# Kernel optimization log

Hardware: AMD Instinct MI355X
Metric: run time of the kernel (lower is better)

The kernel has to match this reference:

```python
import jax, jax.numpy as jnp
import numpy as np

B, S, D, H = 2, 2048, 2048, 16
HD = D // H          # 128, even for RoPE
GS = 0.1             # governance_strength
ROPE_BASE = 10000.0


def _rope_cos_sin(seq_len, dtype):
    # inv_freq over pairs of dims: [HD/2]
    inv_freq = 1.0 / (ROPE_BASE ** (jnp.arange(0, HD, 2, dtype=jnp.float32) / HD))
    t = jnp.arange(seq_len, dtype=jnp.float32)
    freqs = jnp.outer(t, inv_freq)          # [S, HD/2]
    return jnp.cos(freqs).astype(dtype), jnp.sin(freqs).astype(dtype)


def _apply_rope(x, cos, sin):
    # x: [B,H,S,HD]; cos/sin: [S,HD/2] -> broadcast over batch/heads
    x1, x2 = jnp.split(x, 2, axis=-1)
    c = cos[None, None, :, :]
    s = sin[None, None, :, :]
    return jnp.concatenate([x1 * c - x2 * s, x2 * c + x1 * s], axis=-1)


def setup_inputs() -> dict:
    key = jax.random.key(0)
    ks = jax.random.split(key, 8)
    sc = 1.0 / np.sqrt(D)
    return {
        "x": jax.random.normal(ks[0], (B, S, D), jnp.float32),
        "Wq": jax.random.normal(ks[1], (D, D), jnp.float32) * sc,
        "Wk": jax.random.normal(ks[2], (D, D), jnp.float32) * sc,
        "Wv": jax.random.normal(ks[3], (D, D), jnp.float32) * sc,
        "Wo": jax.random.normal(ks[4], (D, D), jnp.float32) * sc,
        "bo": jnp.zeros((D,), jnp.float32),
        "policy_mask": jax.random.uniform(ks[5], (1, H, S, S), jnp.float32),
        "memory_weights": jax.random.uniform(ks[6], (B, 1, 1, S), jnp.float32),
    }


def reference(x, Wq, Wk, Wv, Wo, bo, policy_mask, memory_weights):
    dtype = x.dtype
    scale = HD ** -0.5

    def heads(t):
        return t.reshape(B, S, H, HD).transpose(0, 2, 1, 3)  # [B,H,S,HD]

    q = heads(x @ Wq)
    k = heads(x @ Wk)
    v = heads(x @ Wv)

    cos, sin = _rope_cos_sin(S, dtype)
    q = _apply_rope(q, cos, sin)
    k = _apply_rope(k, cos, sin)

    scores = jnp.einsum("bhqd,bhkd->bhqk", q, k) * scale  # [B,H,S,S]

    # governance bias: policy term + memory-aware log term
    bias = policy_mask * GS + jnp.log1p(memory_weights * GS + 1e-8)
    scores = scores + bias

    # causal mask (no KV cache: kv_len == q_len)
    causal = jnp.tril(jnp.ones((S, S), bool))[None, None]
    scores = jnp.where(causal, scores, jnp.asarray(-1e9, dtype))

    attn = jax.nn.softmax(scores, axis=-1)
    out = jnp.einsum("bhqk,bhkd->bhqd", attn, v)          # [B,H,S,HD]
    out = out.transpose(0, 2, 1, 3).reshape(B, S, D)
    return out @ Wo + bo
```

## Files before the change

### kernel.cpp

```cpp
#include <hip/hip_runtime.h>
#include <hip/hip_bf16.h>
#include <math.h>

#define B_ 2
#define S_ 2048
#define D_ 2048
#define H_ 16
#define HD_ 128
#define NT_ (B_*S_)
#define GS_ 0.1f

typedef _Float16 half8 __attribute__((__vector_size__(16)));
typedef _Float16 half4v __attribute__((__vector_size__(8)));
typedef float f32x4 __attribute__((__vector_size__(16)));

__device__ __forceinline__ void gload_lds16(const void* g, void* s) {
  __builtin_amdgcn_global_load_lds(
      (const __attribute__((address_space(1))) unsigned int*)g,
      (__attribute__((address_space(3))) unsigned int*)s, 16, 0, 0);
}


__global__ void cvt_f32_to_f16(const float* __restrict__ in, _Float16* __restrict__ out, int n4) {
  int i = blockIdx.x * blockDim.x + threadIdx.x;
  if (i >= n4) return;
  float4 v = ((const float4*)in)[i];
  half4v o = { (_Float16)v.x, (_Float16)v.y, (_Float16)v.z, (_Float16)v.w };
  ((half4v*)out)[i] = o;
}

__global__ void transpose_to_f16(const float* __restrict__ in, _Float16* __restrict__ out, int R, int C) {
  __shared__ float t[32][33];
  int c0 = blockIdx.x*32, r0 = blockIdx.y*32;
  int tx = threadIdx.x, ty = threadIdx.y;
#pragma unroll
  for (int j = 0; j < 32; j += 8)
    t[ty+j][tx] = in[(size_t)(r0+ty+j)*C + c0+tx];
  __syncthreads();
#pragma unroll
  for (int j = 0; j < 32; j += 8)
    out[(size_t)(c0+ty+j)*R + r0+tx] = (_Float16)t[tx][ty+j];
}

__global__ void prep_tables(const float* __restrict__ mw, float* __restrict__ cost,
                            float* __restrict__ sint, float* __restrict__ lmw) {
  int t = blockIdx.x*256 + threadIdx.x;
  if (t < S_*64) {
    int s = t >> 6, d = t & 63;
    float inv = (float)pow(10000.0, -(double)(2*d)/(double)HD_);
    float f = (float)s * inv;
    cost[t] = cosf(f);
    sint[t] = sinf(f);
  }
  if (t < B_*S_) lmw[t] = log1pf(mw[t]*GS_ + 1e-8f);
}


template<bool F32OUT>
__global__ __launch_bounds__(256) void gemm_f16(
    const _Float16* __restrict__ A, const _Float16* __restrict__ Bt,
    void* __restrict__ Cout, const float* __restrict__ bias,
    int M, int N, int K)
{
  __shared__ __align__(16) _Float16 As[128*64];
  __shared__ __align__(16) _Float16 Bs[128*64];
  int n0 = blockIdx.x*128, m0 = blockIdx.y*128;
  int tid = threadIdx.x;
  int w = tid >> 6, l = tid & 63;
  int lhi = l >> 4, llo = l & 15;
  int wr = w >> 1, wc = w & 1;
  const f32x4 fz = {0.f,0.f,0.f,0.f};
  f32x4 acc[4][4];
#pragma unroll
  for (int i = 0; i < 4; ++i)
#pragma unroll
    for (int j = 0; j < 4; ++j) acc[i][j] = fz;

  for (int kt = 0; kt < K; kt += 64) {
#pragma unroll
    for (int i = 0; i < 4; ++i) {
      int sid = i*256 + tid;
      int row = sid >> 3;
      int c   = (sid & 7) ^ (row & 7);
      gload_lds16(A  + (size_t)(m0+row)*K + kt + c*8, (char*)As + (size_t)(i*256 + w*64)*16);
      gload_lds16(Bt + (size_t)(n0+row)*K + kt + c*8, (char*)Bs + (size_t)(i*256 + w*64)*16);
    }
    __syncthreads();
#pragma unroll
    for (int kk = 0; kk < 2; ++kk) {
      half8 a[4], b[4];
#pragma unroll
      for (int mi = 0; mi < 4; ++mi) {
        int row = wr*64 + mi*16 + llo;
        int ch = (kk*4 + lhi) ^ (row & 7);
        a[mi] = *(const half8*)((const char*)As + row*128 + ch*16);
      }
#pragma unroll
      for (int ni = 0; ni < 4; ++ni) {
        int row = wc*64 + ni*16 + llo;
        int ch = (kk*4 + lhi) ^ (row & 7);
        b[ni] = *(const half8*)((const char*)Bs + row*128 + ch*16);
      }
#pragma unroll
      for (int mi = 0; mi < 4; ++mi)
#pragma unroll
        for (int ni = 0; ni < 4; ++ni)
          acc[mi][ni] = __builtin_amdgcn_mfma_f32_16x16x32_f16(a[mi], b[ni], acc[mi][ni], 0, 0, 0);
    }
    __syncthreads();
  }
#pragma unroll
  for (int mi = 0; mi < 4; ++mi)
#pragma unroll
    for (int ni = 0; ni < 4; ++ni)
#pragma unroll
      for (int r = 0; r < 4; ++r) {
        int row = m0 + wr*64 + mi*16 + lhi*4 + r;
        int col = n0 + wc*64 + ni*16 + llo;
        if constexpr (F32OUT)
          ((float*)Cout)[(size_t)row*N + col] = acc[mi][ni][r] + bias[col];
        else
          ((_Float16*)Cout)[(size_t)row*N + col] = (_Float16)acc[mi][ni][r];
      }
}

__global__ void rope_qk(const _Float16* __restrict__ qkv, const float* __restrict__ cost,
                        const float* __restrict__ sint, _Float16* __restrict__ Qr,
                        _Float16* __restrict__ Kr) {
  int token = blockIdx.x;
  int b = token >> 11, s = token & (S_-1);
  int t = threadIdx.x;
  int isk = t >> 7, u = t & 127;
  int hh = u >> 3, dd0 = (u & 7)*8;
  const _Float16* src = qkv + (size_t)token*(3*D_) + (size_t)isk*D_ + hh*128;
  half8 a  = *(const half8*)(src + dd0);
  half8 bb = *(const half8*)(src + 64 + dd0);
  half8 lo, hi;
#pragma unroll
  for (int j = 0; j < 8; ++j) {
    float c  = cost[s*64 + dd0 + j];
    float sn = sint[s*64 + dd0 + j];
    float x1 = (float)a[j], x2 = (float)bb[j];
    lo[j] = (_Float16)(x1*c - x2*sn);
    hi[j] = (_Float16)(x2*c + x1*sn);
  }
  _Float16* dst = (isk ? Kr : Qr) + ((size_t)(b*H_ + hh)*S_ + s)*HD_;
  *(half8*)(dst + dd0) = lo;
  *(half8*)(dst + 64 + dd0) = hi;
}

__global__ void v_transpose(const _Float16* __restrict__ qkv, _Float16* __restrict__ Vt) {
  __shared__ _Float16 tile[64][33];
  int st = blockIdx.x*64;
  int dt = blockIdx.y*32;
  int bh = blockIdx.z;
  int b = bh >> 4, h = bh & 15;
  int t = threadIdx.x;
  int s = t >> 2, dc = (t & 3)*8;
  half8 v = *(const half8*)(qkv + (size_t)(b*S_ + st + s)*(3*D_) + 2*D_ + h*128 + dt + dc);
#pragma unroll
  for (int j = 0; j < 8; ++j) tile[s][dc+j] = v[j];
  __syncthreads();
  int d = t >> 3, sc = (t & 7)*8;
  half8 o;
#pragma unroll
  for (int j = 0; j < 8; ++j) o[j] = tile[sc+j][d];
  *(half8*)(Vt + ((size_t)bh*HD_ + dt + d)*S_ + st + sc) = o;
}

__global__ __launch_bounds__(256) void attn_kernel(
    const _Float16* __restrict__ Qr, const _Float16* __restrict__ Kr,
    const _Float16* __restrict__ Vt, const float* __restrict__ policy,
    const float* __restrict__ lmw, _Float16* __restrict__ Ob)
{
  __shared__ __align__(16) _Float16 Kl[64*128];
  __shared__ __align__(16) _Float16 Vl[128*64];
  __shared__ __align__(16) _Float16 Pl[4][16*64];
  int bx = blockIdx.x;
  int qt = (S_/64) - 1 - (bx / (B_*H_));
  int rem = bx % (B_*H_);
  int h = rem >> 1;
  int b = rem & 1;
  int bh = b*H_ + h;
  const _Float16* Qb = Qr + (size_t)bh*S_*HD_;
  const _Float16* Kb = Kr + (size_t)bh*S_*HD_;
  const _Float16* Vb = Vt + (size_t)bh*HD_*S_;
  const float* pol = policy + (size_t)h*S_*S_;
  int tid = threadIdx.x;
  int w = tid >> 6, l = tid & 63;
  int lhi = l >> 4, llo = l & 15;
  int q0 = qt*64 + w*16;

  half8 qf[4];
#pragma unroll
  for (int c = 0; c < 4; ++c)
    qf[c] = *(const half8*)(Qb + (size_t)(q0+llo)*HD_ + c*32 + lhi*8);

  const f32x4 fz = {0.f,0.f,0.f,0.f};
  f32x4 outacc[8];
#pragma unroll
  for (int i = 0; i < 8; ++i) outacc[i] = fz;
  float m_[4], l_[4];
#pragma unroll
  for (int r = 0; r < 4; ++r) { m_[r] = -INFINITY; l_[r] = 0.f; }

  const float scale = 0.08838834764831845f;
  _Float16* Pw = &Pl[w][0];

  for (int t = 0; t <= qt; ++t) {
    int kv0 = t*64;
#pragma unroll
    for (int i = 0; i < 4; ++i) {
      int sid = i*256 + tid;
      int key = sid >> 4;
      int ck = (sid & 15) ^ (key & 7);
      gload_lds16(Kb + (size_t)(kv0+key)*HD_ + ck*8, (char*)Kl + (size_t)(i*256 + w*64)*16);
      int dv = sid >> 3;
      int cv = (sid & 7) ^ (dv & 7);
      gload_lds16(Vb + (size_t)dv*S_ + kv0 + cv*8, (char*)Vl + (size_t)(i*256 + w*64)*16);
    }
    __syncthreads();

    f32x4 sacc[4];
#pragma unroll
    for (int kf = 0; kf < 4; ++kf) sacc[kf] = fz;
#pragma unroll
    for (int kf = 0; kf < 4; ++kf) {
      int key = kf*16 + llo;
#pragma unroll
      for (int c = 0; c < 4; ++c) {
        int ch = (c*4 + lhi) ^ (key & 7);
        half8 kfr = *(const half8*)((const char*)Kl + key*256 + ch*16);
        sacc[kf] = __builtin_amdgcn_mfma_f32_16x16x32_f16(qf[c], kfr, sacc[kf], 0, 0, 0);
      }
    }

    bool diag = (t == qt);
    float lm[4];
#pragma unroll
    for (int kf = 0; kf < 4; ++kf) lm[kf] = lmw[b*S_ + kv0 + kf*16 + llo];
    float pv[4][4];
#pragma unroll
    for (int kf = 0; kf < 4; ++kf) {
      int gk = kv0 + kf*16 + llo;
#pragma unroll
      for (int r = 0; r < 4; ++r) {
        int gq = q0 + lhi*4 + r;
        float v = sacc[kf][r]*scale + pol[(size_t)gq*S_ + gk]*GS_ + lm[kf];
        if (diag && gk > gq) v = -1e9f;
        pv[kf][r] = v;
      }
    }
    float fct[4];
#pragma unroll
    for (int r = 0; r < 4; ++r) {
      float mx = fmaxf(fmaxf(pv[0][r], pv[1][r]), fmaxf(pv[2][r], pv[3][r]));
#pragma unroll
      for (int s = 8; s > 0; s >>= 1) mx = fmaxf(mx, __shfl_xor(mx, s, 16));
      float mnew = fmaxf(m_[r], mx);
      fct[r] = __expf(m_[r] - mnew);
      m_[r] = mnew;
    }
    float rsum[4] = {0.f,0.f,0.f,0.f};
#pragma unroll
    for (int kf = 0; kf < 4; ++kf)
#pragma unroll
      for (int r = 0; r < 4; ++r) {
        float p = __expf(pv[kf][r] - m_[r]);
        pv[kf][r] = p;
        rsum[r] += p;
      }
#pragma unroll
    for (int r = 0; r < 4; ++r) {
      float rs = rsum[r];
#pragma unroll
      for (int s = 8; s > 0; s >>= 1) rs += __shfl_xor(rs, s, 16);
      l_[r] = l_[r]*fct[r] + rs;
    }
#pragma unroll
    for (int i = 0; i < 8; ++i) {
      f32x4 o = outacc[i];
      o[0] *= fct[0]; o[1] *= fct[1]; o[2] *= fct[2]; o[3] *= fct[3];
      outacc[i] = o;
    }
#pragma unroll
    for (int kf = 0; kf < 4; ++kf)
#pragma unroll
      for (int r = 0; r < 4; ++r) {
        int pq = lhi*4 + r, pk = kf*16 + llo;
        int byte = (pq*128 + pk*2) ^ ((pq & 7) << 4);
        *(_Float16*)((char*)Pw + byte) = (_Float16)pv[kf][r];
      }
#pragma unroll
    for (int kc = 0; kc < 2; ++kc) {
      int ch = (kc*4 + lhi) ^ (llo & 7);
      half8 pa = *(const half8*)((const char*)Pw + llo*128 + ch*16);
#pragma unroll
      for (int db = 0; db < 8; ++db) {
        int d = db*16 + llo;
        int chv = (kc*4 + lhi) ^ (d & 7);
        half8 vb = *(const half8*)((const char*)Vl + d*128 + chv*16);
        outacc[db] = __builtin_amdgcn_mfma_f32_16x16x32_f16(pa, vb, outacc[db], 0, 0, 0);
      }
    }
    __syncthreads();
  }
#pragma unroll
  for (int db = 0; db < 8; ++db)
#pragma unroll
    for (int r = 0; r < 4; ++r) {
      int gq = q0 + lhi*4 + r;
      float o = outacc[db][r] / l_[r];
      Ob[((size_t)b*S_ + gq)*D_ + h*HD_ + db*16 + llo] = (_Float16)o;
    }
}


extern "C" void kernel_launch(void* const* d_in, const int* in_sizes, int n_in,
                              void* d_out, int out_size, void* d_ws, size_t ws_size,
                              hipStream_t stream) {
  const float* x   = (const float*)d_in[0];
  const float* Wq  = (const float*)d_in[1];
  const float* Wk  = (const float*)d_in[2];
  const float* Wv  = (const float*)d_in[3];
  const float* Wo  = (const float*)d_in[4];
  const float* bo  = (const float*)d_in[5];
  const float* pol = (const float*)d_in[6];
  const float* mw  = (const float*)d_in[7];
  float* out = (float*)d_out;

  char* p = (char*)d_ws;
  auto take = [&](size_t bytes) { char* r = p; p += (bytes + 255) & ~(size_t)255; return r; };
  _Float16* xb   = (_Float16*)take((size_t)NT_*D_*2);
  _Float16* Wt   = (_Float16*)take((size_t)3*D_*D_*2);
  _Float16* Wot  = (_Float16*)take((size_t)D_*D_*2);
  _Float16* qkv  = (_Float16*)take((size_t)NT_*3*D_*2);
  _Float16* Qr   = (_Float16*)take((size_t)B_*H_*S_*HD_*2);
  _Float16* Kr   = (_Float16*)take((size_t)B_*H_*S_*HD_*2);
  _Float16* Vtb  = (_Float16*)take((size_t)B_*H_*S_*HD_*2);
  _Float16* Ob   = (_Float16*)take((size_t)NT_*D_*2);
  float* cost = (float*)take((size_t)S_*64*4);
  float* sint = (float*)take((size_t)S_*64*4);
  float* lmwb = (float*)take((size_t)B_*S_*4);

  cvt_f32_to_f16<<<(NT_*D_/4 + 255)/256, 256, 0, stream>>>(x, xb, NT_*D_/4);
  transpose_to_f16<<<dim3(64,64), dim3(32,8), 0, stream>>>(Wq, Wt,                    D_, D_);
  transpose_to_f16<<<dim3(64,64), dim3(32,8), 0, stream>>>(Wk, Wt +   (size_t)D_*D_,  D_, D_);
  transpose_to_f16<<<dim3(64,64), dim3(32,8), 0, stream>>>(Wv, Wt + 2*(size_t)D_*D_,  D_, D_);
  transpose_to_f16<<<dim3(64,64), dim3(32,8), 0, stream>>>(Wo, Wot, D_, D_);
  prep_tables<<<512, 256, 0, stream>>>(mw, cost, sint, lmwb);

  gemm_f16<false><<<dim3(3*D_/128, NT_/128), 256, 0, stream>>>(xb, Wt, qkv, nullptr, NT_, 3*D_, D_);
  rope_qk<<<NT_, 256, 0, stream>>>(qkv, cost, sint, Qr, Kr);
  v_transpose<<<dim3(S_/64, HD_/32, B_*H_), 256, 0, stream>>>(qkv, Vtb);
  attn_kernel<<<B_*H_*(S_/64), 256, 0, stream>>>(Qr, Kr, Vtb, pol, lmwb, Ob);
  gemm_f16<true><<<dim3(D_/128, NT_/128), 256, 0, stream>>>(Ob, Wot, out, bo, NT_, D_, D_);
}
```

Baseline: 349.9 us.

## Replace GEMM with 256x128 multi-buffered pipelined kernel and MFMA priority hints

Swaps the 128x128 single-buffered GEMM for a 512-thread 256x128 tile kernel. It uses a 4-slot LDS ring, prefetches two K-steps ahead, waits with explicit vmcnt, and interleaves quadrant MFMA groups with the next loads. It also adds an XCD-aware block swizzle and raises wave priority around MFMA sections, including in the attention kernel. The goal is to hide global-load latency and keep the matrix units busy. The cost is more LDS per block, a larger grid tile and tricky barrier and waitcnt ordering.

```diff
diff --git a/kernel.cpp b/kernel.cpp
--- a/kernel.cpp
+++ b/kernel.cpp
@@ -13,6 +13,8 @@
 typedef _Float16 half8 __attribute__((__vector_size__(16)));
 typedef _Float16 half4v __attribute__((__vector_size__(8)));
 typedef float f32x4 __attribute__((__vector_size__(16)));
+
+#define VMCNT(n) asm volatile("s_waitcnt vmcnt(" #n ")" ::: "memory")
 
 __device__ __forceinline__ void gload_lds16(const void* g, void* s) {
   __builtin_amdgcn_global_load_lds(
@@ -56,65 +58,114 @@
 }
 
 
+#define QUAD(MH,NH) do{ \
+  _Pragma("unroll") for (int dmi=0;dmi<2;++dmi) \
+  _Pragma("unroll") for (int dni=0;dni<2;++dni) \
+  _Pragma("unroll") for (int kk=0;kk<2;++kk) \
+    acc[(MH)*2+dmi][(NH)*2+dni] = __builtin_amdgcn_mfma_f32_16x16x32_f16( \
+        a[dmi][kk], b[(NH)*2+dni][kk], acc[(MH)*2+dmi][(NH)*2+dni],0,0,0); \
+}while(0)
+
 template<bool F32OUT>
-__global__ __launch_bounds__(256) void gemm_f16(
+__global__ __launch_bounds__(512) void gemm256(
     const _Float16* __restrict__ A, const _Float16* __restrict__ Bt,
     void* __restrict__ Cout, const float* __restrict__ bias,
     int M, int N, int K)
 {
-  __shared__ __align__(16) _Float16 As[128*64];
-  __shared__ __align__(16) _Float16 Bs[128*64];
-  int n0 = blockIdx.x*128, m0 = blockIdx.y*128;
+  __shared__ __align__(16) char Ar[4][16384];
+  __shared__ __align__(16) char Br[4][16384];
+  int nwg = gridDim.x*gridDim.y;
+  int bid = blockIdx.y*gridDim.x + blockIdx.x;
+  int swz = ((nwg&7)==0) ? ((bid&7)*(nwg>>3) + (bid>>3)) : bid;
+  int bx = swz % gridDim.x, by = swz / gridDim.x;
+  int n0 = bx*128, m0 = by*256;
   int tid = threadIdx.x;
-  int w = tid >> 6, l = tid & 63;
-  int lhi = l >> 4, llo = l & 15;
-  int wr = w >> 1, wc = w & 1;
+  int w = tid>>6, l = tid&63, lhi = l>>4, llo = l&15;
+  int wr = w>>1, wc = w&1;
+  int nkt = K>>6;
+
+  auto stage = [&](char* dst, const _Float16* src){
+#pragma unroll
+    for (int i=0;i<2;++i){
+      int s = i*512 + tid;
+      int row = s>>3, ch = (s&7)^(row&7);
+      gload_lds16(src + (size_t)row*K + ch*8, dst + i*8192 + w*1024);
+    }
+  };
+  auto stageA = [&](int h, int tt){ stage(Ar[(2*tt+h)&3], A + (size_t)(m0+h*128)*K + (size_t)tt*64); };
+  auto stageB = [&](int tt){ stage(Br[tt&3], Bt + (size_t)n0*K + (size_t)tt*64); };
+
   const f32x4 fz = {0.f,0.f,0.f,0.f};
   f32x4 acc[4][4];
 #pragma unroll
-  for (int i = 0; i < 4; ++i)
-#pragma unroll
-    for (int j = 0; j < 4; ++j) acc[i][j] = fz;
-
-  for (int kt = 0; kt < K; kt += 64) {
-#pragma unroll
-    for (int i = 0; i < 4; ++i) {
-      int sid = i*256 + tid;
-      int row = sid >> 3;
-      int c   = (sid & 7) ^ (row & 7);
-      gload_lds16(A  + (size_t)(m0+row)*K + kt + c*8, (char*)As + (size_t)(i*256 + w*64)*16);
-      gload_lds16(Bt + (size_t)(n0+row)*K + kt + c*8, (char*)Bs + (size_t)(i*256 + w*64)*16);
-    }
-    __syncthreads();
-#pragma unroll
-    for (int kk = 0; kk < 2; ++kk) {
-      half8 a[4], b[4];
-#pragma unroll
-      for (int mi = 0; mi < 4; ++mi) {
-        int row = wr*64 + mi*16 + llo;
-        int ch = (kk*4 + lhi) ^ (row & 7);
-        a[mi] = *(const half8*)((const char*)As + row*128 + ch*16);
-      }
-#pragma unroll
-      for (int ni = 0; ni < 4; ++ni) {
-        int row = wc*64 + ni*16 + llo;
-        int ch = (kk*4 + lhi) ^ (row & 7);
-        b[ni] = *(const half8*)((const char*)Bs + row*128 + ch*16);
-      }
-#pragma unroll
-      for (int mi = 0; mi < 4; ++mi)
-#pragma unroll
-        for (int ni = 0; ni < 4; ++ni)
-          acc[mi][ni] = __builtin_amdgcn_mfma_f32_16x16x32_f16(a[mi], b[ni], acc[mi][ni], 0, 0, 0);
-    }
-    __syncthreads();
+  for (int i=0;i<4;++i)
+#pragma unroll
+    for (int j=0;j<4;++j) acc[i][j] = fz;
+
+  stageB(0); stageA(0,0); stageA(1,0);
+  if (nkt > 1) { stageB(1); stageA(0,1); VMCNT(4); }
+  else         { VMCNT(0); }
+  __builtin_amdgcn_sched_barrier(0);
+  __builtin_amdgcn_s_barrier();
+
+  int hA = wr>>1;
+  int rb = (wr&1)*64;
+
+  for (int t = 0; t < nkt; ++t) {
+    const char* Au = Ar[(2*t+hA)&3];
+    const char* Bu = Br[t&3];
+    half8 a[2][2], b[4][2];
+#pragma unroll
+    for (int dmi=0;dmi<2;++dmi){
+      int rr = rb + dmi*16 + llo;
+#pragma unroll
+      for (int kk=0;kk<2;++kk)
+        a[dmi][kk] = *(const half8*)(Au + rr*128 + (((kk*4+lhi)^(rr&7))<<4));
+    }
+#pragma unroll
+    for (int ni=0;ni<4;++ni){
+      int rn = wc*64 + ni*16 + llo;
+#pragma unroll
+      for (int kk=0;kk<2;++kk)
+        b[ni][kk] = *(const half8*)(Bu + rn*128 + (((kk*4+lhi)^(rn&7))<<4));
+    }
+    if (t+1 < nkt) stageA(1, t+1);
+    __builtin_amdgcn_s_barrier();
+    __builtin_amdgcn_s_setprio(1);
+    QUAD(0,0);
+    __builtin_amdgcn_s_setprio(0);
+    __builtin_amdgcn_s_barrier();
+    if (t+2 < nkt) stageB(t+2);
+    __builtin_amdgcn_s_setprio(1);
+    QUAD(0,1);
+    __builtin_amdgcn_s_setprio(0);
+    __builtin_amdgcn_s_barrier();
+#pragma unroll
+    for (int dmi=0;dmi<2;++dmi){
+      int rr = rb + 32 + dmi*16 + llo;
+#pragma unroll
+      for (int kk=0;kk<2;++kk)
+        a[dmi][kk] = *(const half8*)(Au + rr*128 + (((kk*4+lhi)^(rr&7))<<4));
+    }
+    __builtin_amdgcn_s_setprio(1);
+    QUAD(1,0);
+    __builtin_amdgcn_s_setprio(0);
+    __builtin_amdgcn_s_barrier();
+    if (t+2 < nkt) stageA(0, t+2);
+    __builtin_amdgcn_s_setprio(1);
+    QUAD(1,1);
+    __builtin_amdgcn_s_setprio(0);
+    if (t+2 < nkt) { VMCNT(4); } else { VMCNT(0); }
+    __builtin_amdgcn_sched_barrier(0);
+    __builtin_amdgcn_s_barrier();
   }
-#pragma unroll
-  for (int mi = 0; mi < 4; ++mi)
-#pragma unroll
-    for (int ni = 0; ni < 4; ++ni)
-#pragma unroll
-      for (int r = 0; r < 4; ++r) {
+
+#pragma unroll
+  for (int mi=0;mi<4;++mi)
+#pragma unroll
+    for (int ni=0;ni<4;++ni)
+#pragma unroll
+      for (int r=0;r<4;++r){
         int row = m0 + wr*64 + mi*16 + lhi*4 + r;
         int col = n0 + wc*64 + ni*16 + llo;
         if constexpr (F32OUT)
@@ -224,6 +275,7 @@
     f32x4 sacc[4];
 #pragma unroll
     for (int kf = 0; kf < 4; ++kf) sacc[kf] = fz;
+    __builtin_amdgcn_s_setprio(1);
 #pragma unroll
     for (int kf = 0; kf < 4; ++kf) {
       int key = kf*16 + llo;
@@ -234,6 +286,7 @@
         sacc[kf] = __builtin_amdgcn_mfma_f32_16x16x32_f16(qf[c], kfr, sacc[kf], 0, 0, 0);
       }
     }
+    __builtin_amdgcn_s_setprio(0);
 
     bool diag = (t == qt);
     float lm[4];
@@ -291,6 +344,7 @@
         int byte = (pq*128 + pk*2) ^ ((pq & 7) << 4);
         *(_Float16*)((char*)Pw + byte) = (_Float16)pv[kf][r];
       }
+    __builtin_amdgcn_s_setprio(1);
 #pragma unroll
     for (int kc = 0; kc < 2; ++kc) {
       int ch = (kc*4 + lhi) ^ (llo & 7);
@@ -303,6 +357,7 @@
         outacc[db] = __builtin_amdgcn_mfma_f32_16x16x32_f16(pa, vb, outacc[db], 0, 0, 0);
       }
     }
+    __builtin_amdgcn_s_setprio(0);
     __syncthreads();
   }
 #pragma unroll
@@ -350,9 +405,9 @@
   transpose_to_f16<<<dim3(64,64), dim3(32,8), 0, stream>>>(Wo, Wot, D_, D_);
   prep_tables<<<512, 256, 0, stream>>>(mw, cost, sint, lmwb);
 
-  gemm_f16<false><<<dim3(3*D_/128, NT_/128), 256, 0, stream>>>(xb, Wt, qkv, nullptr, NT_, 3*D_, D_);
+  gemm256<false><<<dim3(3*D_/128, NT_/256), 512, 0, stream>>>(xb, Wt, qkv, nullptr, NT_, 3*D_, D_);
   rope_qk<<<NT_, 256, 0, stream>>>(qkv, cost, sint, Qr, Kr);
   v_transpose<<<dim3(S_/64, HD_/32, B_*H_), 256, 0, stream>>>(qkv, Vtb);
   attn_kernel<<<B_*H_*(S_/64), 256, 0, stream>>>(Qr, Kr, Vtb, pol, lmwb, Ob);
-  gemm_f16<true><<<dim3(D_/128, NT_/128), 256, 0, stream>>>(Ob, Wot, out, bo, NT_, D_, D_);
-}
+  gemm256<true><<<dim3(D_/128, NT_/256), 512, 0, stream>>>(Ob, Wot, out, bo, NT_, D_, D_);
+}
```

Result: slower. 373.5 us (+6.8%).

## Restructure attention to 128-query tiles with 32x32 MFMA and register P

Applied to the files above, without the earlier changes.

The attention kernel now processes 128 queries per block (32 per wave) using 32x32x16 MFMAs and computes S^T so the softmax probabilities can be repacked into PV operands with lane shuffles instead of a round trip through LDS. Q is prescaled once, policy and memory bias are loaded as float4, the online-softmax rescale is skipped when the max grows by at most 8, and output is staged through LDS for coalesced stores. The change doubles K/V reuse per LDS load and removes P shared-memory traffic, at the cost of half as many blocks, more register pressure, and a lazy-rescale threshold that affects numerical behaviour.

```diff
diff --git a/kernel.cpp b/kernel.cpp
--- a/kernel.cpp
+++ b/kernel.cpp
@@ -12,7 +12,9 @@
 
 typedef _Float16 half8 __attribute__((__vector_size__(16)));
 typedef _Float16 half4v __attribute__((__vector_size__(8)));
+typedef _Float16 half2v __attribute__((__vector_size__(4)));
 typedef float f32x4 __attribute__((__vector_size__(16)));
+typedef float f32x16 __attribute__((__vector_size__(64)));
 
 __device__ __forceinline__ void gload_lds16(const void* g, void* s) {
   __builtin_amdgcn_global_load_lds(
@@ -173,11 +175,11 @@
     const _Float16* __restrict__ Vt, const float* __restrict__ policy,
     const float* __restrict__ lmw, _Float16* __restrict__ Ob)
 {
-  __shared__ __align__(16) _Float16 Kl[64*128];
-  __shared__ __align__(16) _Float16 Vl[128*64];
-  __shared__ __align__(16) _Float16 Pl[4][16*64];
+  __shared__ __align__(16) char SMEM[32768];
+  char* Kl = SMEM;
+  char* Vl = SMEM + 16384;
   int bx = blockIdx.x;
-  int qt = (S_/64) - 1 - (bx / (B_*H_));
+  int qb = (S_/128) - 1 - (bx / (B_*H_));
   int rem = bx % (B_*H_);
   int h = rem >> 1;
   int b = rem & 1;
@@ -186,133 +188,171 @@
   const _Float16* Kb = Kr + (size_t)bh*S_*HD_;
   const _Float16* Vb = Vt + (size_t)bh*HD_*S_;
   const float* pol = policy + (size_t)h*S_*S_;
+  const float* lmb = lmw + b*S_;
   int tid = threadIdx.x;
   int w = tid >> 6, l = tid & 63;
-  int lhi = l >> 4, llo = l & 15;
-  int q0 = qt*64 + w*16;
-
-  half8 qf[4];
-#pragma unroll
-  for (int c = 0; c < 4; ++c)
-    qf[c] = *(const half8*)(Qb + (size_t)(q0+llo)*HD_ + c*32 + lhi*8);
-
-  const f32x4 fz = {0.f,0.f,0.f,0.f};
-  f32x4 outacc[8];
-#pragma unroll
-  for (int i = 0; i < 8; ++i) outacc[i] = fz;
-  float m_[4], l_[4];
-#pragma unroll
-  for (int r = 0; r < 4; ++r) { m_[r] = -INFINITY; l_[r] = 0.f; }
+  int l31 = l & 31, lh = l >> 5;
+  int q0 = qb*128 + w*32;
+  int gq = q0 + l31;
 
   const float scale = 0.08838834764831845f;
-  _Float16* Pw = &Pl[w][0];
-
-  for (int t = 0; t <= qt; ++t) {
+  half8 qf[8];
+#pragma unroll
+  for (int ds = 0; ds < 8; ++ds) {
+    half8 qv = *(const half8*)(Qb + (size_t)gq*HD_ + ds*16 + lh*8);
+#pragma unroll
+    for (int e = 0; e < 8; ++e) qv[e] = (_Float16)((float)qv[e] * scale);
+    qf[ds] = qv;
+  }
+
+  f32x16 oacc[4];
+#pragma unroll
+  for (int i = 0; i < 4; ++i)
+#pragma unroll
+    for (int r = 0; r < 16; ++r) oacc[i][r] = 0.f;
+  float m_ = -INFINITY, l_ = 0.f;
+
+  int nt = qb*2 + 2;
+  for (int t = 0; t < nt; ++t) {
     int kv0 = t*64;
 #pragma unroll
     for (int i = 0; i < 4; ++i) {
       int sid = i*256 + tid;
-      int key = sid >> 4;
-      int ck = (sid & 15) ^ (key & 7);
-      gload_lds16(Kb + (size_t)(kv0+key)*HD_ + ck*8, (char*)Kl + (size_t)(i*256 + w*64)*16);
-      int dv = sid >> 3;
-      int cv = (sid & 7) ^ (dv & 7);
-      gload_lds16(Vb + (size_t)dv*S_ + kv0 + cv*8, (char*)Vl + (size_t)(i*256 + w*64)*16);
+      int krow = sid >> 4;
+      int ck = (sid & 15) ^ (krow & 15);
+      gload_lds16(Kb + (size_t)(kv0+krow)*HD_ + ck*8, Kl + (size_t)(i*256 + w*64)*16);
+      int co = (sid & 15) ^ (krow & 15);
+      int dv = krow*2 + (co >> 3);
+      gload_lds16(Vb + (size_t)dv*S_ + kv0 + (co & 7)*8, Vl + (size_t)(i*256 + w*64)*16);
     }
     __syncthreads();
 
-    f32x4 sacc[4];
-#pragma unroll
-    for (int kf = 0; kf < 4; ++kf) sacc[kf] = fz;
-#pragma unroll
-    for (int kf = 0; kf < 4; ++kf) {
-      int key = kf*16 + llo;
-#pragma unroll
-      for (int c = 0; c < 4; ++c) {
-        int ch = (c*4 + lhi) ^ (key & 7);
-        half8 kfr = *(const half8*)((const char*)Kl + key*256 + ch*16);
-        sacc[kf] = __builtin_amdgcn_mfma_f32_16x16x32_f16(qf[c], kfr, sacc[kf], 0, 0, 0);
-      }
-    }
-
-    bool diag = (t == qt);
-    float lm[4];
-#pragma unroll
-    for (int kf = 0; kf < 4; ++kf) lm[kf] = lmw[b*S_ + kv0 + kf*16 + llo];
-    float pv[4][4];
-#pragma unroll
-    for (int kf = 0; kf < 4; ++kf) {
-      int gk = kv0 + kf*16 + llo;
-#pragma unroll
-      for (int r = 0; r < 4; ++r) {
-        int gq = q0 + lhi*4 + r;
-        float v = sacc[kf][r]*scale + pol[(size_t)gq*S_ + gk]*GS_ + lm[kf];
-        if (diag && gk > gq) v = -1e9f;
-        pv[kf][r] = v;
-      }
-    }
-    float fct[4];
-#pragma unroll
-    for (int r = 0; r < 4; ++r) {
-      float mx = fmaxf(fmaxf(pv[0][r], pv[1][r]), fmaxf(pv[2][r], pv[3][r]));
-#pragma unroll
-      for (int s = 8; s > 0; s >>= 1) mx = fmaxf(mx, __shfl_xor(mx, s, 16));
-      float mnew = fmaxf(m_[r], mx);
-      fct[r] = __expf(m_[r] - mnew);
-      m_[r] = mnew;
-    }
-    float rsum[4] = {0.f,0.f,0.f,0.f};
-#pragma unroll
-    for (int kf = 0; kf < 4; ++kf)
-#pragma unroll
-      for (int r = 0; r < 4; ++r) {
-        float p = __expf(pv[kf][r] - m_[r]);
-        pv[kf][r] = p;
-        rsum[r] += p;
-      }
-#pragma unroll
-    for (int r = 0; r < 4; ++r) {
-      float rs = rsum[r];
-#pragma unroll
-      for (int s = 8; s > 0; s >>= 1) rs += __shfl_xor(rs, s, 16);
-      l_[r] = l_[r]*fct[r] + rs;
-    }
-#pragma unroll
-    for (int i = 0; i < 8; ++i) {
-      f32x4 o = outacc[i];
-      o[0] *= fct[0]; o[1] *= fct[1]; o[2] *= fct[2]; o[3] *= fct[3];
-      outacc[i] = o;
-    }
-#pragma unroll
-    for (int kf = 0; kf < 4; ++kf)
-#pragma unroll
-      for (int r = 0; r < 4; ++r) {
-        int pq = lhi*4 + r, pk = kf*16 + llo;
-        int byte = (pq*128 + pk*2) ^ ((pq & 7) << 4);
-        *(_Float16*)((char*)Pw + byte) = (_Float16)pv[kf][r];
-      }
-#pragma unroll
-    for (int kc = 0; kc < 2; ++kc) {
-      int ch = (kc*4 + lhi) ^ (llo & 7);
-      half8 pa = *(const half8*)((const char*)Pw + llo*128 + ch*16);
-#pragma unroll
-      for (int db = 0; db < 8; ++db) {
-        int d = db*16 + llo;
-        int chv = (kc*4 + lhi) ^ (d & 7);
-        half8 vb = *(const half8*)((const char*)Vl + d*128 + chv*16);
-        outacc[db] = __builtin_amdgcn_mfma_f32_16x16x32_f16(pa, vb, outacc[db], 0, 0, 0);
-      }
-    }
+    f32x16 sacc[2];
+#pragma unroll
+    for (int kh = 0; kh < 2; ++kh)
+#pragma unroll
+      for (int r = 0; r < 16; ++r) sacc[kh][r] = 0.f;
+    __builtin_amdgcn_s_setprio(1);
+#pragma unroll
+    for (int kh = 0; kh < 2; ++kh) {
+      const char* kbase = Kl + (kh*32 + l31)*256;
+      int sw = l & 15;
+#pragma unroll
+      for (int ds = 0; ds < 8; ++ds) {
+        half8 kf = *(const half8*)(kbase + (((ds*2 + lh) ^ sw) << 4));
+        sacc[kh] = __builtin_amdgcn_mfma_f32_32x32x16_f16(kf, qf[ds], sacc[kh], 0, 0, 0);
+      }
+    }
+    __builtin_amdgcn_s_setprio(0);
+
+    bool domask = (kv0 + 63 > q0);
+#pragma unroll
+    for (int kh = 0; kh < 2; ++kh) {
+      float po[16], lm_[16];
+#pragma unroll
+      for (int g = 0; g < 4; ++g) {
+        int gk0 = kv0 + kh*32 + g*8 + lh*4;
+        float4 p4 = *(const float4*)(pol + (size_t)gq*S_ + gk0);
+        float4 l4 = *(const float4*)(lmb + gk0);
+        po[g*4+0]=p4.x; po[g*4+1]=p4.y; po[g*4+2]=p4.z; po[g*4+3]=p4.w;
+        lm_[g*4+0]=l4.x; lm_[g*4+1]=l4.y; lm_[g*4+2]=l4.z; lm_[g*4+3]=l4.w;
+      }
+#pragma unroll
+      for (int r = 0; r < 16; ++r) {
+        float v = fmaf(po[r], GS_, sacc[kh][r] + lm_[r]);
+        int gk = kv0 + kh*32 + (r&3) + 8*(r>>2) + 4*lh;
+        if (domask && gk > gq) v = -1e9f;
+        sacc[kh][r] = v;
+      }
+    }
+
+    float mx = -INFINITY;
+#pragma unroll
+    for (int kh = 0; kh < 2; ++kh)
+#pragma unroll
+      for (int r = 0; r < 16; ++r) mx = fmaxf(mx, sacc[kh][r]);
+    mx = fmaxf(mx, __shfl_xor(mx, 32));
+    bool skip = __all(mx - m_ <= 8.0f);
+    if (!skip) {
+      float mnew = fmaxf(m_, mx);
+      float fct = __expf(m_ - mnew);
+      m_ = mnew;
+      l_ *= fct;
+#pragma unroll
+      for (int i = 0; i < 4; ++i)
+#pragma unroll
+        for (int r = 0; r < 16; ++r) oacc[i][r] *= fct;
+    }
+    float rsum = 0.f;
+#pragma unroll
+    for (int kh = 0; kh < 2; ++kh)
+#pragma unroll
+      for (int r = 0; r < 16; ++r) {
+        float pp = __expf(sacc[kh][r] - m_);
+        sacc[kh][r] = pp;
+        rsum += pp;
+      }
+    rsum += __shfl_xor(rsum, 32);
+    l_ += rsum;
+
+    half8 pfrag[4];
+#pragma unroll
+    for (int s = 0; s < 4; ++s) {
+      int kh = s >> 1, rb = (s & 1)*8;
+      unsigned A0 = __builtin_bit_cast(unsigned, __builtin_amdgcn_cvt_pkrtz(sacc[kh][rb+0], sacc[kh][rb+1]));
+      unsigned A1 = __builtin_bit_cast(unsigned, __builtin_amdgcn_cvt_pkrtz(sacc[kh][rb+2], sacc[kh][rb+3]));
+      unsigned B0 = __builtin_bit_cast(unsigned, __builtin_amdgcn_cvt_pkrtz(sacc[kh][rb+4], sacc[kh][rb+5]));
+      unsigned B1 = __builtin_bit_cast(unsigned, __builtin_amdgcn_cvt_pkrtz(sacc[kh][rb+6], sacc[kh][rb+7]));
+      unsigned sA0 = (unsigned)__shfl_xor((int)A0, 32);
+      unsigned sA1 = (unsigned)__shfl_xor((int)A1, 32);
+      unsigned sB0 = (unsigned)__shfl_xor((int)B0, 32);
+      unsigned sB1 = (unsigned)__shfl_xor((int)B1, 32);
+      uint4 uu;
+      uu.x = lh ? sB0 : A0;
+      uu.y = lh ? sB1 : A1;
+      uu.z = lh ? B0  : sA0;
+      uu.w = lh ? B1  : sA1;
+      pfrag[s] = __builtin_bit_cast(half8, uu);
+    }
+
+    __builtin_amdgcn_s_setprio(1);
+#pragma unroll
+    for (int dt = 0; dt < 4; ++dt) {
+      int d = dt*32 + l31;
+      const char* vbase = Vl + (d >> 1)*256;
+      int swv = l31 >> 1;
+      int cbase = (d & 1) << 3;
+#pragma unroll
+      for (int s = 0; s < 4; ++s) {
+        half8 vf = *(const half8*)(vbase + (((cbase + s*2 + lh) ^ swv) << 4));
+        oacc[dt] = __builtin_amdgcn_mfma_f32_32x32x16_f16(vf, pfrag[s], oacc[dt], 0, 0, 0);
+      }
+    }
+    __builtin_amdgcn_s_setprio(0);
     __syncthreads();
   }
-#pragma unroll
-  for (int db = 0; db < 8; ++db)
-#pragma unroll
-    for (int r = 0; r < 4; ++r) {
-      int gq = q0 + lhi*4 + r;
-      float o = outacc[db][r] / l_[r];
-      Ob[((size_t)b*S_ + gq)*D_ + h*HD_ + db*16 + llo] = (_Float16)o;
-    }
+
+  float inv = 1.f / l_;
+  int q = w*32 + l31;
+#pragma unroll
+  for (int dt = 0; dt < 4; ++dt)
+#pragma unroll
+    for (int rq = 0; rq < 4; ++rq) {
+      half4v o4;
+#pragma unroll
+      for (int j = 0; j < 4; ++j) o4[j] = (_Float16)(oacc[dt][rq*4+j] * inv);
+      int off = q*256 + ((dt*64 + rq*16 + lh*8) ^ ((q & 15) << 4));
+      *(half4v*)(SMEM + off) = o4;
+    }
+  __syncthreads();
+  int qr = tid >> 1, hf = tid & 1;
+  size_t gbase = ((size_t)(b*S_ + qb*128 + qr))*D_ + h*128 + hf*64;
+#pragma unroll
+  for (int j = 0; j < 8; ++j) {
+    int c = hf*8 + j;
+    half8 vv = *(const half8*)(SMEM + qr*256 + ((c ^ (qr & 15)) << 4));
+    *(half8*)(Ob + gbase + j*8) = vv;
+  }
 }
 
 
@@ -353,6 +393,6 @@
   gemm_f16<false><<<dim3(3*D_/128, NT_/128), 256, 0, stream>>>(xb, Wt, qkv, nullptr, NT_, 3*D_, D_);
   rope_qk<<<NT_, 256, 0, stream>>>(qkv, cost, sint, Qr, Kr);
   v_transpose<<<dim3(S_/64, HD_/32, B_*H_), 256, 0, stream>>>(qkv, Vtb);
-  attn_kernel<<<B_*H_*(S_/64), 256, 0, stream>>>(Qr, Kr, Vtb, pol, lmwb, Ob);
+  attn_kernel<<<B_*H_*(S_/128), 256, 0, stream>>>(Qr, Kr, Vtb, pol, lmwb, Ob);
   gemm_f16<true><<<dim3(D_/128, NT_/128), 256, 0, stream>>>(Ob, Wot, out, bo, NT_, D_, D_);
 }
```

Measured after the change: 368.6 us. 1.05x slower.
